# Kernel tuning notes

Measured on AMD Instinct MI355X. Metric: run time of the kernel, lower is better.

Reference implementation:

```python
import jax, jax.numpy as jnp
import numpy as np

TEMPERATURE = 0.07
B, D = 8192, 1024


def setup_inputs() -> dict:
    key = jax.random.key(0)
    k1, k2 = jax.random.split(key)
    audio_embeds = jax.random.normal(k1, (B, D), dtype=jnp.float32)
    text_embeds = jax.random.normal(k2, (B, D), dtype=jnp.float32)
    return {"audio_embeds": audio_embeds, "text_embeds": text_embeds}


def _l2norm(x):
    return x / jnp.linalg.norm(x, axis=-1, keepdims=True)


def reference(audio_embeds, text_embeds):
    # InfoNCE(paired) with leave-one-out negatives + self positive is exactly
    # softmax-CE over the full BxB cosine-similarity matrix with diagonal labels.
    a = _l2norm(audio_embeds)  # [B, D]
    t = _l2norm(text_embeds)   # [B, D]
    sim = jnp.einsum("bd,cd->bc", a, t) / TEMPERATURE  # [B, B]
    # audio->text direction: rows of sim, label = diagonal
    loss_a2t = -jnp.mean(jnp.diagonal(jax.nn.log_softmax(sim, axis=1)))
    # text->audio direction: sim of text queries vs audio keys = sim.T
    loss_t2a = -jnp.mean(jnp.diagonal(jax.nn.log_softmax(sim.T, axis=1)))
    return 0.5 * (loss_a2t + loss_t2a)
```

## Files before the change

### kernel.cpp

```cpp
#include <hip/hip_runtime.h>
#include <stdint.h>

#define D_DIM 1024
#define INV_T 14.2857142857142857f
#define QSCALE 32.0f
#define EPI_SCALE (INV_T / (QSCALE * QSCALE))
#define BK 64
#define NT (D_DIM / BK)

typedef __attribute__((ext_vector_type(4))) float f32x4;
typedef __attribute__((ext_vector_type(2))) long lx2;

__global__ __launch_bounds__(256) void norm_diag_kernel(
    const float* __restrict__ A, const float* __restrict__ T,
    unsigned int* __restrict__ An, unsigned int* __restrict__ Tn,
    float* __restrict__ diag)
{
  const int row = blockIdx.x;
  const int tid = threadIdx.x;
  const size_t base = (size_t)row * D_DIM;
  const float4 av = ((const float4*)(A + base))[tid];
  const float4 tv = ((const float4*)(T + base))[tid];
  float sa = av.x*av.x + av.y*av.y + av.z*av.z + av.w*av.w;
  float st = tv.x*tv.x + tv.y*tv.y + tv.z*tv.z + tv.w*tv.w;
  float sd = av.x*tv.x + av.y*tv.y + av.z*tv.z + av.w*tv.w;
  #pragma unroll
  for (int m = 1; m < 64; m <<= 1) {
    sa += __shfl_xor(sa, m, 64);
    st += __shfl_xor(st, m, 64);
    sd += __shfl_xor(sd, m, 64);
  }
  __shared__ float red[3][4];
  const int wid = tid >> 6;
  if ((tid & 63) == 0) { red[0][wid] = sa; red[1][wid] = st; red[2][wid] = sd; }
  __syncthreads();
  sa = red[0][0] + red[0][1] + red[0][2] + red[0][3];
  st = red[1][0] + red[1][1] + red[1][2] + red[1][3];
  sd = red[2][0] + red[2][1] + red[2][2] + red[2][3];
  const float ra = rsqrtf(sa), rt = rsqrtf(st);
  if (tid == 0) diag[row] = sd * ra * rt * INV_T;
  const float qa = ra * QSCALE, qt = rt * QSCALE;
  unsigned int ao = __builtin_amdgcn_cvt_pk_fp8_f32(av.x*qa, av.y*qa, 0, 0);
  ao = __builtin_amdgcn_cvt_pk_fp8_f32(av.z*qa, av.w*qa, ao, 1);
  unsigned int to = __builtin_amdgcn_cvt_pk_fp8_f32(tv.x*qt, tv.y*qt, 0, 0);
  to = __builtin_amdgcn_cvt_pk_fp8_f32(tv.z*qt, tv.w*qt, to, 1);
  const int idx = (tid & ~15) + ((tid >> 1) & 3) * 4 + ((tid >> 3) & 1) * 2 + (tid & 1);
  An[row * 256 + idx] = ao;
  Tn[row * 256 + idx] = to;
}

__device__ __forceinline__ void gload_lds16(const void* g, void* l) {
  __builtin_amdgcn_global_load_lds(
      (const __attribute__((address_space(1))) unsigned int*)g,
      (__attribute__((address_space(3))) unsigned int*)l, 16, 0, 0);
}

#define SBAR asm volatile("s_barrier" ::: "memory")

#define STAGE2(T) do {                                                          \
    const unsigned char* _a = aP + (size_t)(T) * BK;                            \
    const unsigned char* _b = bP + (size_t)(T) * BK;                            \
    const int _bb = ((T) & 1) * 16384;                                          \
    _Pragma("unroll")                                                           \
    for (int _i = 0; _i < 2; ++_i) {                                            \
      const int _ci = _i*256 + tid;                                             \
      const int _r = _ci >> 2, _c = _ci & 3;                                    \
      const size_t _go = (size_t)_r * D_DIM + ((_c ^ ((_r >> 1) & 3)) << 4);    \
      gload_lds16(_a + _go, &lds[_bb + _ci*16]);                                \
      gload_lds16(_b + _go, &lds[_bb + 8192 + _ci*16]);                         \
    }                                                                           \
  } while (0)

__global__ __launch_bounds__(256, 4) void gemm_lse_kernel(
    const unsigned char* __restrict__ An, const unsigned char* __restrict__ Tn,
    float* __restrict__ Srow, float* __restrict__ Scol, int nbc)
{
  __shared__ unsigned char lds[32768];

  const int nwg = gridDim.x;
  const int bid = blockIdx.x;
  const int cpx = nwg >> 3;
  const int swz = (bid & 7) * cpx + (bid >> 3);
  const int brow = swz / nbc;
  const int bcol = swz - brow * nbc;

  const int tid  = threadIdx.x;
  const int lane = tid & 63;
  const int wid  = tid >> 6;
  const int wr   = wid >> 1, wc = wid & 1;
  const int lcol = lane & 15, lrow = lane >> 4;

  const unsigned char* aP = An + (size_t)brow * 128 * D_DIM;
  const unsigned char* bP = Tn + (size_t)bcol * 128 * D_DIM;

  f32x4 acc[4][4] = {};

  STAGE2(0);
  STAGE2(1);
  asm volatile("s_waitcnt vmcnt(4)" ::: "memory");
  SBAR;

  for (int t = 0; t < NT; ++t) {
    const int bb = (t & 1) * 16384;
    lx2 a2[4], b2[4];
    #pragma unroll
    for (int m = 0; m < 4; ++m) {
      const int row = wr*64 + m*16 + lcol;
      const int c = lrow ^ ((row >> 1) & 3);
      a2[m] = *(const lx2*)&lds[bb + row*64 + c*16];
    }
    #pragma unroll
    for (int n = 0; n < 4; ++n) {
      const int row = wc*64 + n*16 + lcol;
      const int c = lrow ^ ((row >> 1) & 3);
      b2[n] = *(const lx2*)&lds[bb + 8192 + row*64 + c*16];
    }
    #pragma unroll
    for (int m = 0; m < 4; ++m)
      #pragma unroll
      for (int n = 0; n < 4; ++n)
        acc[m][n] = __builtin_amdgcn_mfma_f32_16x16x32_fp8_fp8(a2[m][0], b2[n][0], acc[m][n], 0, 0, 0);
    #pragma unroll
    for (int m = 0; m < 4; ++m)
      #pragma unroll
      for (int n = 0; n < 4; ++n)
        acc[m][n] = __builtin_amdgcn_mfma_f32_16x16x32_fp8_fp8(a2[m][1], b2[n][1], acc[m][n], 0, 0, 0);
    SBAR;
    if (t + 2 < NT) {
      STAGE2(t + 2);
      asm volatile("s_waitcnt vmcnt(4)" ::: "memory");
    } else {
      asm volatile("s_waitcnt vmcnt(0)" ::: "memory");
    }
    SBAR;
  }

  float rowsum[4][4];
  float colsum[4];
  #pragma unroll
  for (int m = 0; m < 4; ++m)
    #pragma unroll
    for (int r = 0; r < 4; ++r) rowsum[m][r] = 0.f;
  #pragma unroll
  for (int n = 0; n < 4; ++n) {
    float cs = 0.f;
    #pragma unroll
    for (int m = 0; m < 4; ++m)
      #pragma unroll
      for (int r = 0; r < 4; ++r) {
        const float e = __expf(acc[m][n][r] * EPI_SCALE);
        rowsum[m][r] += e;
        cs += e;
      }
    colsum[n] = cs;
  }
  #pragma unroll
  for (int m = 0; m < 4; ++m)
    #pragma unroll
    for (int r = 0; r < 4; ++r) {
      float v = rowsum[m][r];
      v += __shfl_xor(v, 1, 64);
      v += __shfl_xor(v, 2, 64);
      v += __shfl_xor(v, 4, 64);
      v += __shfl_xor(v, 8, 64);
      if (lcol == 0)
        atomicAdd(&Srow[brow*128 + wr*64 + m*16 + lrow*4 + r], v);
    }
  #pragma unroll
  for (int n = 0; n < 4; ++n) {
    float v = colsum[n];
    v += __shfl_xor(v, 16, 64);
    v += __shfl_xor(v, 32, 64);
    if (lane < 16)
      atomicAdd(&Scol[bcol*128 + wc*64 + n*16 + lcol], v);
  }
}

__global__ __launch_bounds__(256) void loss_kernel(
    const float* __restrict__ Srow, const float* __restrict__ Scol,
    const float* __restrict__ diag, float* __restrict__ out, int B)
{
  float s = 0.f;
  for (int i = threadIdx.x; i < B; i += 256)
    s += 0.5f * (__logf(Srow[i]) + __logf(Scol[i])) - diag[i];
  #pragma unroll
  for (int m = 1; m < 64; m <<= 1) s += __shfl_xor(s, m, 64);
  __shared__ float red[4];
  if ((threadIdx.x & 63) == 0) red[threadIdx.x >> 6] = s;
  __syncthreads();
  if (threadIdx.x == 0) out[0] = (red[0] + red[1] + red[2] + red[3]) / (float)B;
}

extern "C" void kernel_launch(void* const* d_in, const int* in_sizes, int n_in,
                              void* d_out, int out_size, void* d_ws, size_t ws_size,
                              hipStream_t stream) {
  const float* A = (const float*)d_in[0];
  const float* T = (const float*)d_in[1];
  const int B = in_sizes[0] / D_DIM;
  const int nbc = B / 128;

  char* ws = (char*)d_ws;
  unsigned char* An = (unsigned char*)ws;
  unsigned char* Tn = An + (size_t)B * D_DIM;
  float* Srow = (float*)(ws + (size_t)2 * B * D_DIM);
  float* Scol = Srow + B;
  float* diag = Scol + B;

  hipMemsetAsync(Srow, 0, (size_t)2 * B * sizeof(float), stream);
  norm_diag_kernel<<<B, 256, 0, stream>>>(A, T, (unsigned int*)An, (unsigned int*)Tn, diag);
  gemm_lse_kernel<<<nbc * nbc, 256, 0, stream>>>(An, Tn, Srow, Scol, nbc);
  loss_kernel<<<1, 256, 0, stream>>>(Srow, Scol, diag, (float*)d_out, B);
}
```

Baseline: 162.6 us.

## Triple-buffer LDS tiles and double-buffer MFMA fragments in registers

Measured after the change: 165.3 us. No clear change (+1.6%).

```diff
diff --git a/kernel.cpp b/kernel.cpp
--- a/kernel.cpp
+++ b/kernel.cpp
@@ -57,10 +57,10 @@
 
 #define SBAR asm volatile("s_barrier" ::: "memory")
 
-#define STAGE2(T) do {                                                          \
+#define STAGE2(T, BI) do {                                                      \
     const unsigned char* _a = aP + (size_t)(T) * BK;                            \
     const unsigned char* _b = bP + (size_t)(T) * BK;                            \
-    const int _bb = ((T) & 1) * 16384;                                          \
+    const int _bb = (BI) * 16384;                                               \
     _Pragma("unroll")                                                           \
     for (int _i = 0; _i < 2; ++_i) {                                            \
       const int _ci = _i*256 + tid;                                             \
@@ -71,11 +71,44 @@
     }                                                                           \
   } while (0)
 
-__global__ __launch_bounds__(256, 4) void gemm_lse_kernel(
+#define RD(AV, BV, BI) do {                                                     \
+    const int _bb = (BI) * 16384;                                               \
+    _Pragma("unroll")                                                           \
+    for (int _m = 0; _m < 4; ++_m) {                                            \
+      const int _row = wr*64 + _m*16 + lcol;                                    \
+      const int _c = lrow ^ ((_row >> 1) & 3);                                  \
+      AV[_m] = *(const lx2*)&lds[_bb + _row*64 + _c*16];                        \
+    }                                                                           \
+    _Pragma("unroll")                                                           \
+    for (int _n = 0; _n < 4; ++_n) {                                            \
+      const int _row = wc*64 + _n*16 + lcol;                                    \
+      const int _c = lrow ^ ((_row >> 1) & 3);                                  \
+      BV[_n] = *(const lx2*)&lds[_bb + 8192 + _row*64 + _c*16];                 \
+    }                                                                           \
+  } while (0)
+
+#define MFMA16(AV, BV) do {                                                     \
+    __builtin_amdgcn_s_setprio(1);                                              \
+    _Pragma("unroll")                                                           \
+    for (int _m = 0; _m < 4; ++_m)                                              \
+      _Pragma("unroll")                                                         \
+      for (int _n = 0; _n < 4; ++_n)                                            \
+        acc[_m][_n] = __builtin_amdgcn_mfma_f32_16x16x32_fp8_fp8(               \
+            AV[_m][0], BV[_n][0], acc[_m][_n], 0, 0, 0);                        \
+    _Pragma("unroll")                                                           \
+    for (int _m = 0; _m < 4; ++_m)                                              \
+      _Pragma("unroll")                                                         \
+      for (int _n = 0; _n < 4; ++_n)                                            \
+        acc[_m][_n] = __builtin_amdgcn_mfma_f32_16x16x32_fp8_fp8(               \
+            AV[_m][1], BV[_n][1], acc[_m][_n], 0, 0, 0);                        \
+    __builtin_amdgcn_s_setprio(0);                                              \
+  } while (0)
+
+__global__ __launch_bounds__(256, 3) void gemm_lse_kernel(
     const unsigned char* __restrict__ An, const unsigned char* __restrict__ Tn,
     float* __restrict__ Srow, float* __restrict__ Scol, int nbc)
 {
-  __shared__ unsigned char lds[32768];
+  __shared__ unsigned char lds[49152];
 
   const int nwg = gridDim.x;
   const int bid = blockIdx.x;
@@ -94,40 +127,28 @@
   const unsigned char* bP = Tn + (size_t)bcol * 128 * D_DIM;
 
   f32x4 acc[4][4] = {};
-
-  STAGE2(0);
-  STAGE2(1);
+  lx2 aE[4], bE[4], aO[4], bO[4];
+
+  STAGE2(0, 0);
+  STAGE2(1, 1);
+  STAGE2(2, 2);
   asm volatile("s_waitcnt vmcnt(4)" ::: "memory");
   SBAR;
-
+  RD(aE, bE, 0);
+
+  #pragma unroll
   for (int t = 0; t < NT; ++t) {
-    const int bb = (t & 1) * 16384;
-    lx2 a2[4], b2[4];
-    #pragma unroll
-    for (int m = 0; m < 4; ++m) {
-      const int row = wr*64 + m*16 + lcol;
-      const int c = lrow ^ ((row >> 1) & 3);
-      a2[m] = *(const lx2*)&lds[bb + row*64 + c*16];
+    if (t & 1) {
+      if (t + 1 < NT) RD(aE, bE, (t + 1) % 3);
+      MFMA16(aO, bO);
+    } else {
+      if (t + 1 < NT) RD(aO, bO, (t + 1) % 3);
+      MFMA16(aE, bE);
     }
-    #pragma unroll
-    for (int n = 0; n < 4; ++n) {
-      const int row = wc*64 + n*16 + lcol;
-      const int c = lrow ^ ((row >> 1) & 3);
-      b2[n] = *(const lx2*)&lds[bb + 8192 + row*64 + c*16];
-    }
-    #pragma unroll
-    for (int m = 0; m < 4; ++m)
-      #pragma unroll
-      for (int n = 0; n < 4; ++n)
-        acc[m][n] = __builtin_amdgcn_mfma_f32_16x16x32_fp8_fp8(a2[m][0], b2[n][0], acc[m][n], 0, 0, 0);
-    #pragma unroll
-    for (int m = 0; m < 4; ++m)
-      #pragma unroll
-      for (int n = 0; n < 4; ++n)
-        acc[m][n] = __builtin_amdgcn_mfma_f32_16x16x32_fp8_fp8(a2[m][1], b2[n][1], acc[m][n], 0, 0, 0);
+    asm volatile("s_waitcnt lgkmcnt(0)" ::: "memory");
     SBAR;
-    if (t + 2 < NT) {
-      STAGE2(t + 2);
+    if (t + 3 < NT) {
+      STAGE2(t + 3, t % 3);
       asm volatile("s_waitcnt vmcnt(4)" ::: "memory");
     } else {
       asm volatile("s_waitcnt vmcnt(0)" ::: "memory");
```
